# Optimization experiments

Hardware: AMD Instinct MI355X
Metric: run time of the kernel (lower is better)

Reference implementation:

```python
import jax, jax.numpy as jnp
import numpy as np

B, NPG, DEG, D, H, K, NHID, CB = 64, 512, 16, 128, 4, 5, 50, 512
N = B * NPG
E = N * DEG
TAU = 1.0
EPS = 1e-6
BN_SCALE = 1.0 / np.sqrt(1.0 + 1e-5)  # eval-mode BatchNorm, running mean=0 var=1


def _forward(x, edge_index, batch, emb, gin_W1, gin_b1, gin_W2, gin_b2, bn_gamma, bn_beta, part_W1, part_b1, part_W2, part_b2, Wq, Wk, Wv, Wo, gate_W1, gate_b1, gate_W2, gate_b2, codebook, cls_W1, cls_b1, cls_W2, cls_b2, cls_W3, cls_b3):
    # --- GIN stack: h_i <- MLP((1+eps)*h_i + sum_{j->i} h_j), eps=0 ---
    h = emb[x]  # [N, D]
    src, dst = edge_index[0], edge_index[1]
    n_layers = gin_W1.shape[0]
    for l in range(n_layers):
        agg = jax.ops.segment_sum(h[src], dst, num_segments=N)  # scatter-add neighbor messages
        z = h + agg
        z = jax.nn.relu(z @ gin_W1[l] + gin_b1[l]) @ gin_W2[l] + gin_b2[l]
        z = z * (BN_SCALE * bn_gamma[l]) + bn_beta[l]  # eval BN
        h = jax.nn.relu(z) if l < n_layers - 1 else z
    # --- to_dense_batch (equal-size graphs) + soft partitioner ---
    dense = h.reshape(B, NPG, D)
    cl = jax.nn.relu(dense @ part_W1 + part_b1) @ part_W2 + part_b2  # [B,NPG,K]
    S = jax.nn.softmax(cl / TAU, axis=-1)  # soft node->cluster assignment
    cf = jnp.einsum('bnk,bnd->bkd', S, dense) / (S.sum(1)[..., None] + EPS)
    # --- VQ codebook (l2 nearest neighbor, straight-through) ---
    flat = cf.reshape(-1, D)
    d2 = (flat * flat).sum(-1, keepdims=True) - 2.0 * flat @ codebook.T + (codebook * codebook).sum(-1)
    idx = jnp.argmin(d2, axis=-1)
    zq = cf + jax.lax.stop_gradient(codebook[idx].reshape(B, K, D) - cf)
    # --- scatter-mean graph pooling over batch vector ---
    residue = jax.ops.segment_sum(h, batch, num_segments=B) / NPG  # [B,D]
    # --- global cluster attention (4 heads), residue query vs cluster keys ---
    dh = D // H
    q = (residue @ Wq).reshape(B, H, dh)
    k = (zq @ Wk).reshape(B, K, H, dh)
    v = (zq @ Wv).reshape(B, K, H, dh)
    aw = jax.nn.softmax(jnp.einsum('bhd,bkhd->bhk', q, k) / np.sqrt(dh), axis=-1)
    att = jnp.einsum('bhk,bkhd->bhd', aw, v).reshape(B, D) @ Wo
    # --- feature-wise gated fusion ---
    cat = jnp.concatenate([residue, att], axis=-1)
    g = jax.nn.sigmoid(jax.nn.relu(cat @ gate_W1 + gate_b1) @ gate_W2 + gate_b2)
    fused = g * residue + (1.0 - g) * att
    # --- classifier MLP ---
    z1 = jax.nn.relu(fused @ cls_W1 + cls_b1)
    z2 = jax.nn.relu(z1 @ cls_W2 + cls_b2)
    return z2 @ cls_W3 + cls_b3


def setup_inputs():
    key = jax.random.key(0)
    ks = jax.random.split(key, 20)
    def lin(k, i, o):
        return jax.random.normal(k, (i, o), jnp.float32) / np.sqrt(i)
    x = jax.random.randint(ks[0], (N,), 0, 21, dtype=jnp.int32)
    srcn = jnp.repeat(jnp.arange(N, dtype=jnp.int32), DEG)
    dstn = (srcn // NPG) * NPG + jax.random.randint(ks[1], (E,), 0, NPG, dtype=jnp.int32)
    edge_index = jnp.stack([srcn, dstn])
    batch = jnp.repeat(jnp.arange(B, dtype=jnp.int32), NPG)
    return {
        'x': x, 'edge_index': edge_index, 'batch': batch,
        'emb': jax.random.normal(ks[2], (21, D), jnp.float32) * 0.02,
        'gin_W1': jax.random.normal(ks[3], (3, D, 2 * D), jnp.float32) / np.sqrt(D),
        'gin_b1': jnp.zeros((3, 2 * D), jnp.float32),
        'gin_W2': jax.random.normal(ks[4], (3, 2 * D, D), jnp.float32) / np.sqrt(2 * D),
        'gin_b2': jnp.zeros((3, D), jnp.float32),
        'bn_gamma': jnp.ones((3, D), jnp.float32),
        'bn_beta': jnp.zeros((3, D), jnp.float32),
        'part_W1': lin(ks[5], D, NHID), 'part_b1': jnp.zeros((NHID,), jnp.float32),
        'part_W2': lin(ks[6], NHID, K), 'part_b2': jnp.zeros((K,), jnp.float32),
        'Wq': lin(ks[7], D, D), 'Wk': lin(ks[8], D, D), 'Wv': lin(ks[9], D, D), 'Wo': lin(ks[10], D, D),
        'gate_W1': lin(ks[11], 2 * D, D // 2), 'gate_b1': jnp.zeros((D // 2,), jnp.float32),
        'gate_W2': lin(ks[12], D // 2, D), 'gate_b2': jnp.zeros((D,), jnp.float32),
        'codebook': jax.random.normal(ks[13], (CB, D), jnp.float32) * 0.1,
        'cls_W1': lin(ks[14], D, 4 * D), 'cls_b1': jnp.zeros((4 * D,), jnp.float32),
        'cls_W2': lin(ks[15], 4 * D, 2 * D), 'cls_b2': jnp.zeros((2 * D,), jnp.float32),
        'cls_W3': lin(ks[16], 2 * D, 2), 'cls_b3': jnp.zeros((2,), jnp.float32),
    }


def reference(x, edge_index, batch, emb, gin_W1, gin_b1, gin_W2, gin_b2, bn_gamma, bn_beta, part_W1, part_b1, part_W2, part_b2, Wq, Wk, Wv, Wo, gate_W1, gate_b1, gate_W2, gate_b2, codebook, cls_W1, cls_b1, cls_W2, cls_b2, cls_W3, cls_b3):
    return _forward(x, edge_index, batch, emb, gin_W1, gin_b1, gin_W2, gin_b2, bn_gamma, bn_beta, part_W1, part_b1, part_W2, part_b2, Wq, Wk, Wv, Wo, gate_W1, gate_b1, gate_W2, gate_b2, codebook, cls_W1, cls_b1, cls_W2, cls_b2, cls_W3, cls_b3)
```

## Files before the change

kernel.cpp:

```cpp
#include <hip/hip_runtime.h>

constexpr int B_    = 64;
constexpr int NPG_  = 512;
constexpr int D_    = 128;
constexpr int K_    = 5;
constexpr int NHID_ = 50;
constexpr int CB_   = 512;
constexpr int N_    = B_ * NPG_;
constexpr int E_    = N_ * 16;
constexpr float BN_SCALE_ = 0.99999500003749969f;
constexpr float EPS_ = 1e-6f;

typedef __attribute__((ext_vector_type(8))) short bf16x8_t;
typedef __attribute__((ext_vector_type(4))) float f32x4_t;

__device__ __forceinline__ unsigned short f2bf(float x) {
    unsigned int u = __float_as_uint(x);
    unsigned int r = (u + 0x7FFFu + ((u >> 16) & 1u)) >> 16;
    return (unsigned short)r;
}
__device__ __forceinline__ float bf2f(unsigned short b) {
    return __uint_as_float(((unsigned int)b) << 16);
}

__device__ __forceinline__ f32x4_t mfma3(bf16x8_t a0, bf16x8_t a1,
                                         bf16x8_t b0, bf16x8_t b1, f32x4_t acc) {
    acc = __builtin_amdgcn_mfma_f32_16x16x32_bf16(a1, b0, acc, 0, 0, 0);
    acc = __builtin_amdgcn_mfma_f32_16x16x32_bf16(a0, b1, acc, 0, 0, 0);
    acc = __builtin_amdgcn_mfma_f32_16x16x32_bf16(a0, b0, acc, 0, 0, 0);
    return acc;
}

__global__ __launch_bounds__(512) void k_prepcsr(
    const int* __restrict__ dst, int* __restrict__ rowptr, int* __restrict__ col,
    const float* __restrict__ gw1, const float* __restrict__ gw2,
    unsigned short* __restrict__ w1h, unsigned short* __restrict__ w1l,
    unsigned short* __restrict__ w2h, unsigned short* __restrict__ w2l,
    const float* __restrict__ pw1src,
    unsigned short* __restrict__ pw1h, unsigned short* __restrict__ pw1l) {
    __shared__ int cnt[512];
    __shared__ int sc[512];
    __shared__ short dstS[8192];
    int b = blockIdx.x, t = threadIdx.x;
    if (b >= 448) {
        int e2 = (b - 448) * 512 + t;
        int k = e2 >> 6, n = e2 & 63;
        float v = (n < NHID_) ? pw1src[k * NHID_ + n] : 0.f;
        unsigned short h0 = f2bf(v);
        int o = ((((n >> 4) * 4 + (k >> 5)) * 64 + ((k >> 3) & 3) * 16 + (n & 15)) << 3) + (k & 7);
        pw1h[o] = h0; pw1l[o] = f2bf(v - bf2f(h0));
        return;
    }
    if (b >= 64) {
        int e = (b - 64) * 512 + t;
        int layer = e >> 16, rem = e & 65535;
        if (rem < 32768) {
            int k = rem >> 8, n = rem & 255;
            float v = gw1[layer * 32768 + rem];
            unsigned short h0 = f2bf(v);
            int o = layer * 32768 +
                    ((((n >> 4) * 4 + (k >> 5)) * 64 + ((k >> 3) & 3) * 16 + (n & 15)) << 3) + (k & 7);
            w1h[o] = h0; w1l[o] = f2bf(v - bf2f(h0));
        } else {
            int rr = rem - 32768;
            int c = rr >> 7, n = rr & 127;
            float v = gw2[layer * 32768 + rr];
            unsigned short h0 = f2bf(v);
            int o = layer * 32768 +
                    ((((n >> 4) * 8 + (c >> 5)) * 64 + ((c >> 3) & 3) * 16 + (n & 15)) << 3) + (c & 7);
            w2h[o] = h0; w2l[o] = f2bf(v - bf2f(h0));
        }
        return;
    }
    int g = b;
    int base = g * 8192;
    cnt[t] = 0;
    __syncthreads();
    for (int i = t; i < 8192; i += 512) {
        int d = dst[base + i] & 511;
        dstS[i] = (short)d;
        atomicAdd(&cnt[d], 1);
    }
    __syncthreads();
    int c0 = cnt[t];
    sc[t] = c0;
    __syncthreads();
    for (int off = 1; off < 512; off <<= 1) {
        int v = sc[t];
        int add = (t >= off) ? sc[t - off] : 0;
        __syncthreads();
        sc[t] = v + add;
        __syncthreads();
    }
    int excl = sc[t] - c0;
    rowptr[g * 512 + t] = base + excl;
    cnt[t] = excl;
    if (g == 0 && t == 0) rowptr[N_] = E_;
    __syncthreads();
    for (int i = t; i < 8192; i += 512) {
        int d = dstS[i];
        int p = atomicAdd(&cnt[d], 1);
        col[base + p] = g * 512 + (i >> 4);
    }
}

constexpr int LDH = 264;
constexpr int COLCAP = 1024;
template<int L0, int LAST>
__global__ __launch_bounds__(512, LAST ? 4 : 8) void k_gin(
    const float* __restrict__ hIn, const int* __restrict__ rowptr,
    const int* __restrict__ col,
    const int* __restrict__ xIdx, const float* __restrict__ emb,
    const unsigned short* __restrict__ w1h, const unsigned short* __restrict__ w1l,
    const unsigned short* __restrict__ w2h, const unsigned short* __restrict__ w2l,
    const float* __restrict__ b1, const float* __restrict__ b2,
    const float* __restrict__ gamma, const float* __restrict__ beta,
    int relu_out, float* __restrict__ hOut,
    const unsigned short* __restrict__ pw1h, const unsigned short* __restrict__ pw1l,
    const float* __restrict__ pb1,
    const float* __restrict__ pW2, const float* __restrict__ pb2,
    float* __restrict__ pacc, float* __restrict__ pss, float* __restrict__ prs) {
    __shared__ int colS[COLCAP];
    __shared__ __attribute__((aligned(16))) unsigned short bufH[32 * LDH];
    __shared__ __attribute__((aligned(16))) unsigned short bufL[32 * LDH];
    __shared__ float embS[L0 ? 21 * 128 : 1];
    __shared__ int xS[L0 ? 512 : 1];
    __shared__ float ltS[LAST ? 32 * 5 : 1];
    int i = blockIdx.x;
    int xcd = i & 7;
    int slot = i >> 3;
    int g = (slot >> 4) * 8 + xcd;
    int tile = slot & 15;
    int rowBase = g * 512 + tile * 32;
    int t = threadIdx.x;
    int w = t >> 6, l = t & 63;
    int l15 = l & 15, quad = l >> 4;
    int half = l >> 5, lane4 = l & 31;

    int ebase = rowptr[rowBase];
    int ecnt  = rowptr[rowBase + 32] - ebase;
    bool inLds = (ecnt <= COLCAP);
    if (inLds)
        for (int j = t; j < ecnt; j += 512) colS[j] = col[ebase + j];
    if constexpr (L0) {
        for (int j = t; j < 21 * 128; j += 512) embS[j] = emb[j];
        if (t < 512) xS[t] = xIdx[(rowBase & ~511) + t];
    }
    __syncthreads();

    const f32x4_t* h4 = (const f32x4_t*)hIn;
    #pragma unroll
    for (int jj = 0; jj < 2; jj++) {
        int row = w * 4 + half * 2 + jj;
        int node = rowBase + row;
        int beg = rowptr[node], end = rowptr[node + 1];
        f32x4_t a;
        if constexpr (L0)
            a = *(const f32x4_t*)&embS[xS[node & 511] * 128 + lane4 * 4];
        else
            a = h4[node * 32 + lane4];
        int e = beg;
        for (; e + 8 <= end; e += 8) {
            int c[8];
            #pragma unroll
            for (int u = 0; u < 8; u++)
                c[u] = inLds ? colS[e - ebase + u] : col[e + u];
            f32x4_t p[8];
            #pragma unroll
            for (int u = 0; u < 8; u++) {
                if constexpr (L0)
                    p[u] = *(const f32x4_t*)&embS[xS[c[u] & 511] * 128 + lane4 * 4];
                else
                    p[u] = h4[c[u] * 32 + lane4];
            }
            f32x4_t s01 = p[0] + p[1], s23 = p[2] + p[3];
            f32x4_t s45 = p[4] + p[5], s67 = p[6] + p[7];
            a += (s01 + s23) + (s45 + s67);
        }
        for (; e < end; e++) {
            int c = inLds ? colS[e - ebase] : col[e];
            f32x4_t p;
            if constexpr (L0)
                p = *(const f32x4_t*)&embS[xS[c & 511] * 128 + lane4 * 4];
            else
                p = h4[c * 32 + lane4];
            a += p;
        }
        unsigned short h0 = f2bf(a[0]), h1 = f2bf(a[1]), h2s = f2bf(a[2]), h3 = f2bf(a[3]);
        uint2 hv, lv;
        hv.x = (unsigned)h0 | ((unsigned)h1 << 16);
        hv.y = (unsigned)h2s | ((unsigned)h3 << 16);
        lv.x = (unsigned)f2bf(a[0] - bf2f(h0)) | ((unsigned)f2bf(a[1] - bf2f(h1)) << 16);
        lv.y = (unsigned)f2bf(a[2] - bf2f(h2s)) | ((unsigned)f2bf(a[3] - bf2f(h3)) << 16);
        *(uint2*)&bufH[row * LDH + lane4 * 4] = hv;
        *(uint2*)&bufL[row * LDH + lane4 * 4] = lv;
    }
    __syncthreads();

    f32x4_t acc[2][2];
    #pragma unroll
    for (int nt = 0; nt < 2; nt++) {
        float bb = b1[w * 32 + nt * 16 + l15];
        acc[0][nt] = (f32x4_t){bb, bb, bb, bb};
        acc[1][nt] = (f32x4_t){bb, bb, bb, bb};
    }
    #pragma unroll
    for (int kk = 0; kk < 4; kk++) {
        bf16x8_t ah[2], al[2];
        #pragma unroll
        for (int mt = 0; mt < 2; mt++) {
            int addr = (mt * 16 + l15) * LDH + kk * 32 + quad * 8;
            ah[mt] = *(const bf16x8_t*)&bufH[addr];
            al[mt] = *(const bf16x8_t*)&bufL[addr];
        }
        #pragma unroll
        for (int nt = 0; nt < 2; nt++) {
            int n16 = w * 2 + nt;
            int ga = (((n16 * 4 + kk) * 64 + l) << 3);
            bf16x8_t bh = *(const bf16x8_t*)&w1h[ga];
            bf16x8_t bl = *(const bf16x8_t*)&w1l[ga];
            acc[0][nt] = mfma3(ah[0], al[0], bh, bl, acc[0][nt]);
            acc[1][nt] = mfma3(ah[1], al[1], bh, bl, acc[1][nt]);
        }
    }
    __syncthreads();
    #pragma unroll
    for (int mt = 0; mt < 2; mt++)
        #pragma unroll
        for (int nt = 0; nt < 2; nt++) {
            int colL = w * 32 + nt * 16 + l15;
            #pragma unroll
            for (int r = 0; r < 4; r++) {
                int row = mt * 16 + quad * 4 + r;
                float v = fmaxf(acc[mt][nt][r], 0.f);
                unsigned short h0 = f2bf(v);
                bufH[row * LDH + colL] = h0;
                bufL[row * LDH + colL] = f2bf(v - bf2f(h0));
            }
        }
    __syncthreads();

    f32x4_t acc2[2];
    {
        float bb = b2[w * 16 + l15];
        acc2[0] = (f32x4_t){bb, bb, bb, bb};
        acc2[1] = (f32x4_t){bb, bb, bb, bb};
    }
    #pragma unroll
    for (int kkG = 0; kkG < 8; kkG++) {
        bf16x8_t ah[2], al[2];
        #pragma unroll
        for (int mt = 0; mt < 2; mt++) {
            int addr = (mt * 16 + l15) * LDH + kkG * 32 + quad * 8;
            ah[mt] = *(const bf16x8_t*)&bufH[addr];
            al[mt] = *(const bf16x8_t*)&bufL[addr];
        }
        int ga = (((w * 8 + kkG) * 64 + l) << 3);
        bf16x8_t bh = *(const bf16x8_t*)&w2h[ga];
        bf16x8_t bl = *(const bf16x8_t*)&w2l[ga];
        acc2[0] = mfma3(ah[0], al[0], bh, bl, acc2[0]);
        acc2[1] = mfma3(ah[1], al[1], bh, bl, acc2[1]);
    }
    int colC = w * 16 + l15;
    float gm = BN_SCALE_ * gamma[colC];
    float be = beta[colC];
    if constexpr (!LAST) {
        #pragma unroll
        for (int mt = 0; mt < 2; mt++)
            #pragma unroll
            for (int r = 0; r < 4; r++) {
                int row = mt * 16 + quad * 4 + r;
                float v = fmaf(acc2[mt][r], gm, be);
                if (relu_out) v = fmaxf(v, 0.f);
                hOut[(size_t)(rowBase + row) * 128 + colC] = v;
            }
    } else {
        __syncthreads();
        #pragma unroll
        for (int mt = 0; mt < 2; mt++)
            #pragma unroll
            for (int r = 0; r < 4; r++) {
                int row = mt * 16 + quad * 4 + r;
                float v = fmaf(acc2[mt][r], gm, be);
                unsigned short h0 = f2bf(v);
                bufH[row * LDH + colC] = h0;
                bufL[row * LDH + colC] = f2bf(v - bf2f(h0));
            }
        __syncthreads();
        {
            int mtw = w >> 2, ntw = w & 3;
            int ocol = ntw * 16 + l15;
            float bb = (ocol < NHID_) ? pb1[ocol] : 0.f;
            f32x4_t acch = (f32x4_t){bb, bb, bb, bb};
            #pragma unroll
            for (int kk = 0; kk < 4; kk++) {
                int addr = (mtw * 16 + l15) * LDH + kk * 32 + quad * 8;
                bf16x8_t ah = *(const bf16x8_t*)&bufH[addr];
                bf16x8_t al = *(const bf16x8_t*)&bufL[addr];
                int ga = (((ntw * 4 + kk) * 64 + l) << 3);
                bf16x8_t bh = *(const bf16x8_t*)&pw1h[ga];
                bf16x8_t bl = *(const bf16x8_t*)&pw1l[ga];
                acch = mfma3(ah, al, bh, bl, acch);
            }
            float* htF = (float*)bufH;
            #pragma unroll
            for (int r = 0; r < 4; r++) {
                int row = mtw * 16 + quad * 4 + r;
                htF[row * 132 + 64 + ocol] = fmaxf(acch[r], 0.f);
            }
        }
        __syncthreads();
        {
            float* htF = (float*)bufH;
            if (t < 160) {
                int row = t / 5, kk5 = t % 5;
                float a = pb2[kk5];
                for (int c = 0; c < NHID_; c++)
                    a = fmaf(htF[row * 132 + 64 + c], pW2[c * K_ + kk5], a);
                ltS[row * 5 + kk5] = a;
            }
        }
        __syncthreads();
        if (t < 32) {
            float l0 = ltS[t*5], l1 = ltS[t*5+1], l2 = ltS[t*5+2],
                  l3 = ltS[t*5+3], l4 = ltS[t*5+4];
            float m = fmaxf(fmaxf(fmaxf(l0, l1), fmaxf(l2, l3)), l4);
            float e0 = expf(l0 - m), e1 = expf(l1 - m), e2 = expf(l2 - m),
                  e3 = expf(l3 - m), e4 = expf(l4 - m);
            float inv = 1.0f / (e0 + e1 + e2 + e3 + e4);
            ltS[t*5]   = e0*inv; ltS[t*5+1] = e1*inv; ltS[t*5+2] = e2*inv;
            ltS[t*5+3] = e3*inv; ltS[t*5+4] = e4*inv;
        }
        __syncthreads();
        int cIdx = g * 16 + tile;
        for (int j = t; j < 640; j += 512) {
            int k = j >> 7, d = j & 127;
            float a = 0;
            #pragma unroll 8
            for (int r = 0; r < 32; r++) {
                float zv = bf2f(bufH[r * LDH + d]) + bf2f(bufL[r * LDH + d]);
                a = fmaf(ltS[r * 5 + k], zv, a);
            }
            pacc[((size_t)cIdx * 5 + k) * 128 + d] = a;
        }
        if (t < 128) {
            float a = 0;
            #pragma unroll 8
            for (int r = 0; r < 32; r++)
                a += bf2f(bufH[r * LDH + t]) + bf2f(bufL[r * LDH + t]);
            prs[cIdx * 128 + t] = a;
        } else if (t < 133) {
            int k = t - 128;
            float a = 0;
            #pragma unroll 8
            for (int r = 0; r < 32; r++) a += ltS[r * 5 + k];
            pss[cIdx * 5 + k] = a;
        }
    }
}

__global__ __launch_bounds__(1024) void k_tail(
    const float* __restrict__ pacc, const float* __restrict__ pss,
    const float* __restrict__ prs, const float* __restrict__ cbk,
    const float* __restrict__ Wq, const float* __restrict__ Wk,
    const float* __restrict__ Wv, const float* __restrict__ Wo,
    const float* __restrict__ gW1, const float* __restrict__ gb1,
    const float* __restrict__ gW2, const float* __restrict__ gb2,
    const float* __restrict__ cW1, const float* __restrict__ cb1,
    const float* __restrict__ cW2, const float* __restrict__ cb2,
    const float* __restrict__ cW3, const float* __restrict__ cb3,
    float* __restrict__ out) {
    __shared__ float cfS[5 * 128];
    __shared__ float zqS[5 * 128];
    __shared__ float catS[256];
    __shared__ float qS[128];
    __shared__ float kS[5 * 128];
    __shared__ float vS[5 * 128];
    __shared__ float awS[20];
    __shared__ float att1S[128];
    __shared__ float attP[4][128];
    __shared__ float g1P[8][64];
    __shared__ float g1S[64];
    __shared__ float g2P[4][128];
    __shared__ float fusedS[128];
    __shared__ float z1P[2][512];
    __shared__ float z1S[512];
    __shared__ float z2P[4][256];
    __shared__ float bd5[5][512];
    __shared__ int   bi5[5][512];
    __shared__ int   idxS[5];
    __shared__ float red[8];

    int g = blockIdx.x, t = threadIdx.x;

    if (t < 768) {
        int c = t >> 7, d = t & 127;
        if (c == 5) {
            float rs = 0;
            #pragma unroll
            for (int ch = 0; ch < 16; ch++) rs += prs[(g * 16 + ch) * 128 + d];
            catS[d] = rs * (1.0f / 512.0f);
        } else {
            float acc = 0, ss = 0;
            #pragma unroll
            for (int ch = 0; ch < 16; ch++) {
                int blk = g * 16 + ch;
                acc += pacc[((size_t)blk * 5 + c) * 128 + d];
                ss  += pss[blk * 5 + c];
            }
            cfS[c * 128 + d] = acc / (ss + EPS_);
        }
    }
    __syncthreads();

    if (t < 512) {
        const float4* cj = (const float4*)(cbk + (size_t)t * 128);
        float d2[5] = {0, 0, 0, 0, 0};
        #pragma unroll 8
        for (int q4 = 0; q4 < 32; q4++) {
            float4 c4 = cj[q4];
            #pragma unroll
            for (int k = 0; k < 5; k++) {
                float4 f4 = ((const float4*)(cfS + k * 128))[q4];
                float dx = f4.x - c4.x, dy = f4.y - c4.y;
                float dz = f4.z - c4.z, dw = f4.w - c4.w;
                d2[k] = fmaf(dx, dx, d2[k]); d2[k] = fmaf(dy, dy, d2[k]);
                d2[k] = fmaf(dz, dz, d2[k]); d2[k] = fmaf(dw, dw, d2[k]);
            }
        }
        #pragma unroll
        for (int k = 0; k < 5; k++) { bd5[k][t] = d2[k]; bi5[k][t] = t; }
    }
    __syncthreads();
    for (int s = 256; s > 0; s >>= 1) {
        if (t < s) {
            #pragma unroll
            for (int k = 0; k < 5; k++) {
                float bo = bd5[k][t + s]; int io = bi5[k][t + s];
                if (bo < bd5[k][t] || (bo == bd5[k][t] && io < bi5[k][t])) {
                    bd5[k][t] = bo; bi5[k][t] = io;
                }
            }
        }
        __syncthreads();
    }
    if (t < 5) idxS[t] = bi5[t][0];
    __syncthreads();
    if (t < 640) zqS[t] = cbk[(size_t)idxS[t >> 7] * 128 + (t & 127)];
    __syncthreads();

    for (int o = t; o < 1408; o += 1024) {
        const float* Arow; const float* W; int dcol;
        if (o < 128)      { Arow = catS;                     W = Wq; dcol = o; }
        else if (o < 768) { Arow = &zqS[((o - 128) >> 7) * 128]; W = Wk; dcol = (o - 128) & 127; }
        else              { Arow = &zqS[((o - 768) >> 7) * 128]; W = Wv; dcol = (o - 768) & 127; }
        float a0 = 0, a1 = 0, a2 = 0, a3 = 0;
        for (int kk = 0; kk < 128; kk += 4) {
            a0 = fmaf(Arow[kk],     W[kk * 128 + dcol],       a0);
            a1 = fmaf(Arow[kk + 1], W[(kk + 1) * 128 + dcol], a1);
            a2 = fmaf(Arow[kk + 2], W[(kk + 2) * 128 + dcol], a2);
            a3 = fmaf(Arow[kk + 3], W[(kk + 3) * 128 + dcol], a3);
        }
        float acc = (a0 + a1) + (a2 + a3);
        if (o < 128)      qS[o] = acc;
        else if (o < 768) kS[o - 128] = acc;
        else              vS[o - 768] = acc;
    }
    __syncthreads();

    if (t < 20) {
        int hh = t / 5, j = t % 5;
        float s = 0;
        #pragma unroll
        for (int d2 = 0; d2 < 32; d2++)
            s = fmaf(qS[hh * 32 + d2], kS[j * 128 + hh * 32 + d2], s);
        awS[t] = s * 0.17677669529663687f;
    }
    __syncthreads();
    if (t < 4) {
        float m = -1e30f;
        for (int j = 0; j < 5; j++) m = fmaxf(m, awS[t * 5 + j]);
        float e[5], sum = 0;
        for (int j = 0; j < 5; j++) { e[j] = expf(awS[t * 5 + j] - m); sum += e[j]; }
        for (int j = 0; j < 5; j++) awS[t * 5 + j] = e[j] / sum;
    }
    __syncthreads();
    if (t < 128) {
        int hh = t >> 5;
        float a = 0;
        #pragma unroll
        for (int j = 0; j < 5; j++) a = fmaf(awS[hh * 5 + j], vS[j * 128 + t], a);
        att1S[t] = a;
    }
    __syncthreads();
    if (t < 512) {
        int o = t & 127, kq = t >> 7;
        float a0 = 0, a1 = 0;
        #pragma unroll 8
        for (int i = 0; i < 32; i += 2) {
            int kk = kq * 32 + i;
            a0 = fmaf(att1S[kk],     Wo[kk * 128 + o],       a0);
            a1 = fmaf(att1S[kk + 1], Wo[(kk + 1) * 128 + o], a1);
        }
        attP[kq][o] = a0 + a1;
    }
    __syncthreads();
    if (t < 128) catS[128 + t] = attP[0][t] + attP[1][t] + attP[2][t] + attP[3][t];
    __syncthreads();

    if (t < 512) {
        int o = t & 63, kq = t >> 6;
        float a0 = 0, a1 = 0;
        #pragma unroll 8
        for (int i = 0; i < 32; i += 2) {
            int kk = kq * 32 + i;
            a0 = fmaf(catS[kk],     gW1[kk * 64 + o],       a0);
            a1 = fmaf(catS[kk + 1], gW1[(kk + 1) * 64 + o], a1);
        }
        g1P[kq][o] = a0 + a1;
    }
    __syncthreads();
    if (t < 64) {
        float a = gb1[t];
        #pragma unroll
        for (int q = 0; q < 8; q++) a += g1P[q][t];
        g1S[t] = fmaxf(a, 0.f);
    }
    __syncthreads();
    if (t < 512) {
        int o = t & 127, kq = t >> 7;
        float a0 = 0, a1 = 0;
        #pragma unroll 8
        for (int i = 0; i < 16; i += 2) {
            int kk = kq * 16 + i;
            a0 = fmaf(g1S[kk],     gW2[kk * 128 + o],       a0);
            a1 = fmaf(g1S[kk + 1], gW2[(kk + 1) * 128 + o], a1);
        }
        g2P[kq][o] = a0 + a1;
    }
    __syncthreads();
    if (t < 128) {
        float a = gb2[t] + g2P[0][t] + g2P[1][t] + g2P[2][t] + g2P[3][t];
        float gv = 1.f / (1.f + expf(-a));
        fusedS[t] = gv * catS[t] + (1.f - gv) * catS[128 + t];
    }
    __syncthreads();

    {
        int o = t & 511, kq = t >> 9;
        float a0 = 0, a1 = 0, a2 = 0, a3 = 0;
        #pragma unroll 4
        for (int i = 0; i < 64; i += 4) {
            int kk = kq * 64 + i;
            a0 = fmaf(fusedS[kk],     cW1[kk * 512 + o],       a0);
            a1 = fmaf(fusedS[kk + 1], cW1[(kk + 1) * 512 + o], a1);
            a2 = fmaf(fusedS[kk + 2], cW1[(kk + 2) * 512 + o], a2);
            a3 = fmaf(fusedS[kk + 3], cW1[(kk + 3) * 512 + o], a3);
        }
        z1P[kq][o] = (a0 + a1) + (a2 + a3);
    }
    __syncthreads();
    if (t < 512) z1S[t] = fmaxf(z1P[0][t] + z1P[1][t] + cb1[t], 0.f);
    __syncthreads();
    {
        int o = t & 255, kq = t >> 8;
        float a0 = 0, a1 = 0, a2 = 0, a3 = 0;
        #pragma unroll 4
        for (int i = 0; i < 128; i += 4) {
            int kk = kq * 128 + i;
            a0 = fmaf(z1S[kk],     cW2[kk * 256 + o],       a0);
            a1 = fmaf(z1S[kk + 1], cW2[(kk + 1) * 256 + o], a1);
            a2 = fmaf(z1S[kk + 2], cW2[(kk + 2) * 256 + o], a2);
            a3 = fmaf(z1S[kk + 3], cW2[(kk + 3) * 256 + o], a3);
        }
        z2P[kq][o] = (a0 + a1) + (a2 + a3);
    }
    __syncthreads();
    if (t < 256) {
        float zv = fmaxf(z2P[0][t] + z2P[1][t] + z2P[2][t] + z2P[3][t] + cb2[t], 0.f);
        float p0 = zv * cW3[t * 2];
        float p1 = zv * cW3[t * 2 + 1];
        #pragma unroll
        for (int off = 32; off > 0; off >>= 1) {
            p0 += __shfl_down(p0, off, 64);
            p1 += __shfl_down(p1, off, 64);
        }
        int wv = t >> 6;
        if ((t & 63) == 0) { red[wv * 2] = p0; red[wv * 2 + 1] = p1; }
    }
    __syncthreads();
    if (t < 2)
        out[g * 2 + t] = cb3[t] + red[t] + red[2 + t] + red[4 + t] + red[6 + t];
}

extern "C" void kernel_launch(void* const* d_in, const int* in_sizes, int n_in,
                              void* d_out, int out_size, void* d_ws, size_t ws_size,
                              hipStream_t stream) {
    const int*   x          = (const int*)d_in[0];
    const int*   edge_index = (const int*)d_in[1];
    const float* emb      = (const float*)d_in[3];
    const float* gin_W1   = (const float*)d_in[4];
    const float* gin_b1   = (const float*)d_in[5];
    const float* gin_W2   = (const float*)d_in[6];
    const float* gin_b2   = (const float*)d_in[7];
    const float* bn_gamma = (const float*)d_in[8];
    const float* bn_beta  = (const float*)d_in[9];
    const float* part_W1  = (const float*)d_in[10];
    const float* part_b1  = (const float*)d_in[11];
    const float* part_W2  = (const float*)d_in[12];
    const float* part_b2  = (const float*)d_in[13];
    const float* Wq       = (const float*)d_in[14];
    const float* Wk       = (const float*)d_in[15];
    const float* Wv       = (const float*)d_in[16];
    const float* Wo       = (const float*)d_in[17];
    const float* gate_W1  = (const float*)d_in[18];
    const float* gate_b1  = (const float*)d_in[19];
    const float* gate_W2  = (const float*)d_in[20];
    const float* gate_b2  = (const float*)d_in[21];
    const float* codebook = (const float*)d_in[22];
    const float* cls_W1   = (const float*)d_in[23];
    const float* cls_b1   = (const float*)d_in[24];
    const float* cls_W2   = (const float*)d_in[25];
    const float* cls_b2   = (const float*)d_in[26];
    const float* cls_W3   = (const float*)d_in[27];
    const float* cls_b3   = (const float*)d_in[28];

    const int* dstp = edge_index + E_;

    char* w = (char*)d_ws;
    float* hA = (float*)w;  w += (size_t)N_ * D_ * 4;
    float* hB = (float*)w;  w += (size_t)N_ * D_ * 4;
    int* rowptr = (int*)w;  w += (size_t)(N_ + 4) * 4;
    int* col    = (int*)w;  w += (size_t)E_ * 4;
    unsigned short* w1h = (unsigned short*)w;  w += (size_t)3 * 32768 * 2;
    unsigned short* w1l = (unsigned short*)w;  w += (size_t)3 * 32768 * 2;
    unsigned short* w2h = (unsigned short*)w;  w += (size_t)3 * 32768 * 2;
    unsigned short* w2l = (unsigned short*)w;  w += (size_t)3 * 32768 * 2;
    unsigned short* pw1h = (unsigned short*)w;  w += (size_t)8192 * 2;
    unsigned short* pw1l = (unsigned short*)w;  w += (size_t)8192 * 2;
    float* pacc = (float*)w;  w += (size_t)1024 * 5 * 128 * 4;
    float* pss  = (float*)w;  w += (size_t)1024 * 5 * 4;
    float* prs  = (float*)w;  w += (size_t)1024 * 128 * 4;

    k_prepcsr<<<464, 512, 0, stream>>>(dstp, rowptr, col,
                                       gin_W1, gin_W2, w1h, w1l, w2h, w2l,
                                       part_W1, pw1h, pw1l);

    k_gin<1, 0><<<1024, 512, 0, stream>>>(
        hA, rowptr, col, x, emb,
        w1h, w1l, w2h, w2l,
        gin_b1, gin_b2, bn_gamma, bn_beta, 1, hB,
        nullptr, nullptr, nullptr, nullptr, nullptr, nullptr, nullptr, nullptr);
    k_gin<0, 0><<<1024, 512, 0, stream>>>(
        hB, rowptr, col, x, emb,
        w1h + 32768, w1l + 32768, w2h + 32768, w2l + 32768,
        gin_b1 + 256, gin_b2 + 128, bn_gamma + 128, bn_beta + 128, 1, hA,
        nullptr, nullptr, nullptr, nullptr, nullptr, nullptr, nullptr, nullptr);
    k_gin<0, 1><<<1024, 512, 0, stream>>>(
        hA, rowptr, col, x, emb,
        w1h + 65536, w1l + 65536, w2h + 65536, w2l + 65536,
        gin_b1 + 512, gin_b2 + 256, bn_gamma + 256, bn_beta + 256, 0, nullptr,
        pw1h, pw1l, part_b1, part_W2, part_b2, pacc, pss, prs);

    k_tail<<<B_, 1024, 0, stream>>>(pacc, pss, prs, codebook,
                                    Wq, Wk, Wv, Wo,
                                    gate_W1, gate_b1, gate_W2, gate_b2,
                                    cls_W1, cls_b1, cls_W2, cls_b2, cls_W3, cls_b3,
                                    (float*)d_out);
}
```

Measured before the change: 250.8 us.

## Halve GIN row tile to 16 rows with 256-thread blocks and read embeddings from global

Each GIN block now handles 16 rows with 4 waves instead of 32 rows with 8 waves, and the grid doubles to 2048 blocks. The MFMA work is re-split so each wave covers more output columns over a single M tile. The partial-reduction buffers and the tail kernel are resized to match. Layer 0 no longer stages the embedding table in LDS and gathers it from global/cache instead. The aim is more resident blocks and less LDS per block, at the cost of loading each weight fragment for half as many rows and of more partial sums to combine.

```diff
diff --git a/kernel.cpp b/kernel.cpp
--- a/kernel.cpp
+++ b/kernel.cpp
@@ -105,9 +105,9 @@
 }
 
 constexpr int LDH = 264;
-constexpr int COLCAP = 1024;
+constexpr int COLCAP = 640;
 template<int L0, int LAST>
-__global__ __launch_bounds__(512, LAST ? 4 : 8) void k_gin(
+__global__ __launch_bounds__(256, 8) void k_gin(
     const float* __restrict__ hIn, const int* __restrict__ rowptr,
     const int* __restrict__ col,
     const int* __restrict__ xIdx, const float* __restrict__ emb,
@@ -121,34 +121,32 @@
     const float* __restrict__ pW2, const float* __restrict__ pb2,
     float* __restrict__ pacc, float* __restrict__ pss, float* __restrict__ prs) {
     __shared__ int colS[COLCAP];
-    __shared__ __attribute__((aligned(16))) unsigned short bufH[32 * LDH];
-    __shared__ __attribute__((aligned(16))) unsigned short bufL[32 * LDH];
-    __shared__ float embS[L0 ? 21 * 128 : 1];
+    __shared__ __attribute__((aligned(16))) unsigned short bufH[16 * LDH];
+    __shared__ __attribute__((aligned(16))) unsigned short bufL[16 * LDH];
     __shared__ int xS[L0 ? 512 : 1];
-    __shared__ float ltS[LAST ? 32 * 5 : 1];
+    __shared__ float ltS[LAST ? 16 * 5 : 1];
     int i = blockIdx.x;
     int xcd = i & 7;
     int slot = i >> 3;
-    int g = (slot >> 4) * 8 + xcd;
-    int tile = slot & 15;
-    int rowBase = g * 512 + tile * 32;
+    int g = (slot >> 5) * 8 + xcd;
+    int tile = slot & 31;
+    int rowBase = g * 512 + tile * 16;
     int t = threadIdx.x;
     int w = t >> 6, l = t & 63;
     int l15 = l & 15, quad = l >> 4;
     int half = l >> 5, lane4 = l & 31;
 
     int ebase = rowptr[rowBase];
-    int ecnt  = rowptr[rowBase + 32] - ebase;
+    int ecnt  = rowptr[rowBase + 16] - ebase;
     bool inLds = (ecnt <= COLCAP);
     if (inLds)
-        for (int j = t; j < ecnt; j += 512) colS[j] = col[ebase + j];
-    if constexpr (L0) {
-        for (int j = t; j < 21 * 128; j += 512) embS[j] = emb[j];
-        if (t < 512) xS[t] = xIdx[(rowBase & ~511) + t];
-    }
+        for (int j = t; j < ecnt; j += 256) colS[j] = col[ebase + j];
+    if constexpr (L0)
+        for (int j = t; j < 512; j += 256) xS[j] = xIdx[(rowBase & ~511) + j];
     __syncthreads();
 
     const f32x4_t* h4 = (const f32x4_t*)hIn;
+    const f32x4_t* e4 = (const f32x4_t*)emb;
     #pragma unroll
     for (int jj = 0; jj < 2; jj++) {
         int row = w * 4 + half * 2 + jj;
@@ -156,7 +154,7 @@
         int beg = rowptr[node], end = rowptr[node + 1];
         f32x4_t a;
         if constexpr (L0)
-            a = *(const f32x4_t*)&embS[xS[node & 511] * 128 + lane4 * 4];
+            a = e4[xS[node & 511] * 32 + lane4];
         else
             a = h4[node * 32 + lane4];
         int e = beg;
@@ -169,7 +167,7 @@
             #pragma unroll
             for (int u = 0; u < 8; u++) {
                 if constexpr (L0)
-                    p[u] = *(const f32x4_t*)&embS[xS[c[u] & 511] * 128 + lane4 * 4];
+                    p[u] = e4[xS[c[u] & 511] * 32 + lane4];
                 else
                     p[u] = h4[c[u] * 32 + lane4];
             }
@@ -181,7 +179,7 @@
             int c = inLds ? colS[e - ebase] : col[e];
             f32x4_t p;
             if constexpr (L0)
-                p = *(const f32x4_t*)&embS[xS[c & 511] * 128 + lane4 * 4];
+                p = e4[xS[c & 511] * 32 + lane4];
             else
                 p = h4[c * 32 + lane4];
             a += p;
@@ -197,107 +195,101 @@
     }
     __syncthreads();
 
-    f32x4_t acc[2][2];
+    f32x4_t acc1[4];
     #pragma unroll
-    for (int nt = 0; nt < 2; nt++) {
-        float bb = b1[w * 32 + nt * 16 + l15];
-        acc[0][nt] = (f32x4_t){bb, bb, bb, bb};
-        acc[1][nt] = (f32x4_t){bb, bb, bb, bb};
+    for (int nt = 0; nt < 4; nt++) {
+        float bb = b1[(w * 4 + nt) * 16 + l15];
+        acc1[nt] = (f32x4_t){bb, bb, bb, bb};
     }
     #pragma unroll
     for (int kk = 0; kk < 4; kk++) {
-        bf16x8_t ah[2], al[2];
-        #pragma unroll
-        for (int mt = 0; mt < 2; mt++) {
-            int addr = (mt * 16 + l15) * LDH + kk * 32 + quad * 8;
-            ah[mt] = *(const bf16x8_t*)&bufH[addr];
-            al[mt] = *(const bf16x8_t*)&bufL[addr];
-        }
-        #pragma unroll
-        for (int nt = 0; nt < 2; nt++) {
-            int n16 = w * 2 + nt;
+        int addr = l15 * LDH + kk * 32 + quad * 8;
+        bf16x8_t ah = *(const bf16x8_t*)&bufH[addr];
+        bf16x8_t al = *(const bf16x8_t*)&bufL[addr];
+        #pragma unroll
+        for (int nt = 0; nt < 4; nt++) {
+            int n16 = w * 4 + nt;
             int ga = (((n16 * 4 + kk) * 64 + l) << 3);
             bf16x8_t bh = *(const bf16x8_t*)&w1h[ga];
             bf16x8_t bl = *(const bf16x8_t*)&w1l[ga];
-            acc[0][nt] = mfma3(ah[0], al[0], bh, bl, acc[0][nt]);
-            acc[1][nt] = mfma3(ah[1], al[1], bh, bl, acc[1][nt]);
+            acc1[nt] = mfma3(ah, al, bh, bl, acc1[nt]);
         }
     }
     __syncthreads();
     #pragma unroll
-    for (int mt = 0; mt < 2; mt++)
-        #pragma unroll
-        for (int nt = 0; nt < 2; nt++) {
-            int colL = w * 32 + nt * 16 + l15;
-            #pragma unroll
-            for (int r = 0; r < 4; r++) {
-                int row = mt * 16 + quad * 4 + r;
-                float v = fmaxf(acc[mt][nt][r], 0.f);
-                unsigned short h0 = f2bf(v);
-                bufH[row * LDH + colL] = h0;
-                bufL[row * LDH + colL] = f2bf(v - bf2f(h0));
-            }
-        }
+    for (int nt = 0; nt < 4; nt++) {
+        int colL = (w * 4 + nt) * 16 + l15;
+        #pragma unroll
+        for (int r = 0; r < 4; r++) {
+            int row = quad * 4 + r;
+            float v = fmaxf(acc1[nt][r], 0.f);
+            unsigned short h0 = f2bf(v);
+            bufH[row * LDH + colL] = h0;
+            bufL[row * LDH + colL] = f2bf(v - bf2f(h0));
+        }
+    }
     __syncthreads();
 
     f32x4_t acc2[2];
-    {
-        float bb = b2[w * 16 + l15];
-        acc2[0] = (f32x4_t){bb, bb, bb, bb};
-        acc2[1] = (f32x4_t){bb, bb, bb, bb};
+    #pragma unroll
+    for (int nt2 = 0; nt2 < 2; nt2++) {
+        float bb = b2[(w * 2 + nt2) * 16 + l15];
+        acc2[nt2] = (f32x4_t){bb, bb, bb, bb};
     }
     #pragma unroll
     for (int kkG = 0; kkG < 8; kkG++) {
-        bf16x8_t ah[2], al[2];
-        #pragma unroll
-        for (int mt = 0; mt < 2; mt++) {
-            int addr = (mt * 16 + l15) * LDH + kkG * 32 + quad * 8;
-            ah[mt] = *(const bf16x8_t*)&bufH[addr];
-            al[mt] = *(const bf16x8_t*)&bufL[addr];
-        }
-        int ga = (((w * 8 + kkG) * 64 + l) << 3);
-        bf16x8_t bh = *(const bf16x8_t*)&w2h[ga];
-        bf16x8_t bl = *(const bf16x8_t*)&w2l[ga];
-        acc2[0] = mfma3(ah[0], al[0], bh, bl, acc2[0]);
-        acc2[1] = mfma3(ah[1], al[1], bh, bl, acc2[1]);
-    }
-    int colC = w * 16 + l15;
-    float gm = BN_SCALE_ * gamma[colC];
-    float be = beta[colC];
+        int addr = l15 * LDH + kkG * 32 + quad * 8;
+        bf16x8_t ah = *(const bf16x8_t*)&bufH[addr];
+        bf16x8_t al = *(const bf16x8_t*)&bufL[addr];
+        #pragma unroll
+        for (int nt2 = 0; nt2 < 2; nt2++) {
+            int ga = ((((w * 2 + nt2) * 8 + kkG) * 64 + l) << 3);
+            bf16x8_t bh = *(const bf16x8_t*)&w2h[ga];
+            bf16x8_t bl = *(const bf16x8_t*)&w2l[ga];
+            acc2[nt2] = mfma3(ah, al, bh, bl, acc2[nt2]);
+        }
+    }
     if constexpr (!LAST) {
         #pragma unroll
-        for (int mt = 0; mt < 2; mt++)
+        for (int nt2 = 0; nt2 < 2; nt2++) {
+            int colC = (w * 2 + nt2) * 16 + l15;
+            float gm = BN_SCALE_ * gamma[colC];
+            float be = beta[colC];
             #pragma unroll
             for (int r = 0; r < 4; r++) {
-                int row = mt * 16 + quad * 4 + r;
-                float v = fmaf(acc2[mt][r], gm, be);
+                int row = quad * 4 + r;
+                float v = fmaf(acc2[nt2][r], gm, be);
                 if (relu_out) v = fmaxf(v, 0.f);
                 hOut[(size_t)(rowBase + row) * 128 + colC] = v;
             }
+        }
     } else {
         __syncthreads();
         #pragma unroll
-        for (int mt = 0; mt < 2; mt++)
+        for (int nt2 = 0; nt2 < 2; nt2++) {
+            int colC = (w * 2 + nt2) * 16 + l15;
+            float gm = BN_SCALE_ * gamma[colC];
+            float be = beta[colC];
             #pragma unroll
             for (int r = 0; r < 4; r++) {
-                int row = mt * 16 + quad * 4 + r;
-                float v = fmaf(acc2[mt][r], gm, be);
+                int row = quad * 4 + r;
+                float v = fmaf(acc2[nt2][r], gm, be);
                 unsigned short h0 = f2bf(v);
                 bufH[row * LDH + colC] = h0;
                 bufL[row * LDH + colC] = f2bf(v - bf2f(h0));
             }
+        }
         __syncthreads();
         {
-            int mtw = w >> 2, ntw = w & 3;
-            int ocol = ntw * 16 + l15;
+            int ocol = w * 16 + l15;
             float bb = (ocol < NHID_) ? pb1[ocol] : 0.f;
             f32x4_t acch = (f32x4_t){bb, bb, bb, bb};
             #pragma unroll
             for (int kk = 0; kk < 4; kk++) {
-                int addr = (mtw * 16 + l15) * LDH + kk * 32 + quad * 8;
+                int addr = l15 * LDH + kk * 32 + quad * 8;
                 bf16x8_t ah = *(const bf16x8_t*)&bufH[addr];
                 bf16x8_t al = *(const bf16x8_t*)&bufL[addr];
-                int ga = (((ntw * 4 + kk) * 64 + l) << 3);
+                int ga = (((w * 4 + kk) * 64 + l) << 3);
                 bf16x8_t bh = *(const bf16x8_t*)&pw1h[ga];
                 bf16x8_t bl = *(const bf16x8_t*)&pw1l[ga];
                 acch = mfma3(ah, al, bh, bl, acch);
@@ -305,14 +297,14 @@
             float* htF = (float*)bufH;
             #pragma unroll
             for (int r = 0; r < 4; r++) {
-                int row = mtw * 16 + quad * 4 + r;
+                int row = quad * 4 + r;
                 htF[row * 132 + 64 + ocol] = fmaxf(acch[r], 0.f);
             }
         }
         __syncthreads();
         {
             float* htF = (float*)bufH;
-            if (t < 160) {
+            if (t < 80) {
                 int row = t / 5, kk5 = t % 5;
                 float a = pb2[kk5];
                 for (int c = 0; c < NHID_; c++)
@@ -321,7 +313,7 @@
             }
         }
         __syncthreads();
-        if (t < 32) {
+        if (t < 16) {
             float l0 = ltS[t*5], l1 = ltS[t*5+1], l2 = ltS[t*5+2],
                   l3 = ltS[t*5+3], l4 = ltS[t*5+4];
             float m = fmaxf(fmaxf(fmaxf(l0, l1), fmaxf(l2, l3)), l4);
@@ -332,12 +324,12 @@
             ltS[t*5+3] = e3*inv; ltS[t*5+4] = e4*inv;
         }
         __syncthreads();
-        int cIdx = g * 16 + tile;
-        for (int j = t; j < 640; j += 512) {
+        int cIdx = g * 32 + tile;
+        for (int j = t; j < 640; j += 256) {
             int k = j >> 7, d = j & 127;
             float a = 0;
             #pragma unroll 8
-            for (int r = 0; r < 32; r++) {
+            for (int r = 0; r < 16; r++) {
                 float zv = bf2f(bufH[r * LDH + d]) + bf2f(bufL[r * LDH + d]);
                 a = fmaf(ltS[r * 5 + k], zv, a);
             }
@@ -346,14 +338,14 @@
         if (t < 128) {
             float a = 0;
             #pragma unroll 8
-            for (int r = 0; r < 32; r++)
+            for (int r = 0; r < 16; r++)
                 a += bf2f(bufH[r * LDH + t]) + bf2f(bufL[r * LDH + t]);
             prs[cIdx * 128 + t] = a;
         } else if (t < 133) {
             int k = t - 128;
             float a = 0;
             #pragma unroll 8
-            for (int r = 0; r < 32; r++) a += ltS[r * 5 + k];
+            for (int r = 0; r < 16; r++) a += ltS[r * 5 + k];
             pss[cIdx * 5 + k] = a;
         }
     }
@@ -398,13 +390,13 @@
         if (c == 5) {
             float rs = 0;
             #pragma unroll
-            for (int ch = 0; ch < 16; ch++) rs += prs[(g * 16 + ch) * 128 + d];
+            for (int ch = 0; ch < 32; ch++) rs += prs[(g * 32 + ch) * 128 + d];
             catS[d] = rs * (1.0f / 512.0f);
         } else {
             float acc = 0, ss = 0;
             #pragma unroll
-            for (int ch = 0; ch < 16; ch++) {
-                int blk = g * 16 + ch;
+            for (int ch = 0; ch < 32; ch++) {
+                int blk = g * 32 + ch;
                 acc += pacc[((size_t)blk * 5 + c) * 128 + d];
                 ss  += pss[blk * 5 + c];
             }
@@ -638,25 +630,25 @@
     unsigned short* w2l = (unsigned short*)w;  w += (size_t)3 * 32768 * 2;
     unsigned short* pw1h = (unsigned short*)w;  w += (size_t)8192 * 2;
     unsigned short* pw1l = (unsigned short*)w;  w += (size_t)8192 * 2;
-    float* pacc = (float*)w;  w += (size_t)1024 * 5 * 128 * 4;
-    float* pss  = (float*)w;  w += (size_t)1024 * 5 * 4;
-    float* prs  = (float*)w;  w += (size_t)1024 * 128 * 4;
+    float* pacc = (float*)w;  w += (size_t)2048 * 5 * 128 * 4;
+    float* pss  = (float*)w;  w += (size_t)2048 * 5 * 4;
+    float* prs  = (float*)w;  w += (size_t)2048 * 128 * 4;
 
     k_prepcsr<<<464, 512, 0, stream>>>(dstp, rowptr, col,
                                        gin_W1, gin_W2, w1h, w1l, w2h, w2l,
                                        part_W1, pw1h, pw1l);
 
-    k_gin<1, 0><<<1024, 512, 0, stream>>>(
+    k_gin<1, 0><<<2048, 256, 0, stream>>>(
         hA, rowptr, col, x, emb,
         w1h, w1l, w2h, w2l,
         gin_b1, gin_b2, bn_gamma, bn_beta, 1, hB,
         nullptr, nullptr, nullptr, nullptr, nullptr, nullptr, nullptr, nullptr);
-    k_gin<0, 0><<<1024, 512, 0, stream>>>(
+    k_gin<0, 0><<<2048, 256, 0, stream>>>(
         hB, rowptr, col, x, emb,
         w1h + 32768, w1l + 32768, w2h + 32768, w2l + 32768,
         gin_b1 + 256, gin_b2 + 128, bn_gamma + 128, bn_beta + 128, 1, hA,
         nullptr, nullptr, nullptr, nullptr, nullptr, nullptr, nullptr, nullptr);
-    k_gin<0, 1><<<1024, 512, 0, stream>>>(
+    k_gin<0, 1><<<2048, 256, 0, stream>>>(
         hA, rowptr, col, x, emb,
         w1h + 65536, w1l + 65536, w2h + 65536, w2l + 65536,
         gin_b1 + 512, gin_b2 + 256, bn_gamma + 256, bn_beta + 256, 0, nullptr,
```

Measured after the change: 274.3 us. 9.4% more time.
